# Optimization experiments

Measured on AMD Instinct MI355X. Metric: run time of the kernel, lower is better.

The kernel has to match this reference:

```python
import jax, jax.numpy as jnp
import numpy as np
from jax import lax

B, N, D, H, K = 8, 1024, 384, 6, 7
HD = D // H
EPS = 1e-5


def layer_norm(x, g, b):
    m = jnp.mean(x, axis=-1, keepdims=True)
    v = jnp.mean(jnp.square(x - m), axis=-1, keepdims=True)
    return (x - m) * lax.rsqrt(v + EPS) * g + b


def setup_inputs() -> dict:
    key = jax.random.key(0)
    ks = jax.random.split(key, 12)
    s = 0.02
    return {
        "x": jax.random.normal(ks[0], (B, N, D), jnp.float32),
        "qkv_w": jax.random.normal(ks[1], (3 * D, D), jnp.float32) * s,
        "qkv_b": jnp.zeros((3 * D,), jnp.float32),
        "proj_w": jax.random.normal(ks[2], (D, D), jnp.float32) * s,
        "proj_b": jnp.zeros((D,), jnp.float32),
        "t_before": jnp.eye(H, dtype=jnp.float32) + jax.random.normal(ks[3], (H, H), jnp.float32) * 0.01,
        "t_after": jnp.eye(H, dtype=jnp.float32) + jax.random.normal(ks[4], (H, H), jnp.float32) * 0.01,
        "dw_w": jax.random.normal(ks[5], (D, 1, K), jnp.float32) * s,
        "dw_b": jnp.zeros((D,), jnp.float32),
        "mlp_ln_g": jnp.ones((D,), jnp.float32),
        "mlp_ln_b": jnp.zeros((D,), jnp.float32),
        "norm1_g": jnp.ones((D,), jnp.float32),
        "norm1_b": jnp.zeros((D,), jnp.float32),
        "norm2_g": jnp.ones((D,), jnp.float32),
        "norm2_b": jnp.zeros((D,), jnp.float32),
        "fc1_w": jax.random.normal(ks[6], (4 * D, D), jnp.float32) * s,
        "fc1_b": jnp.zeros((4 * D,), jnp.float32),
        "fc2_w": jax.random.normal(ks[7], (D, 4 * D), jnp.float32) * s,
        "fc2_b": jnp.zeros((D,), jnp.float32),
    }


def reference(x, qkv_w, qkv_b, proj_w, proj_b, t_before, t_after, dw_w, dw_b,
              mlp_ln_g, mlp_ln_b, norm1_g, norm1_b, norm2_g, norm2_b,
              fc1_w, fc1_b, fc2_w, fc2_b):
    # ---- attention branch ----
    h = layer_norm(x, norm1_g, norm1_b)
    qkv = h @ qkv_w.T + qkv_b                                  # (B,N,3D)
    qkv = qkv.reshape(B, N, 3, H, HD).transpose(2, 0, 3, 1, 4)  # (3,B,H,N,hd)
    q, k, v = qkv[0], qkv[1], qkv[2]
    scale = HD ** -0.5
    scores = jnp.einsum('bhnd,bhmd->bhnm', q, k) * scale        # (B,H,N,N)
    scores = jnp.einsum('gh,bhnm->bgnm', t_before, scores)       # head-mix pre-softmax
    probs = jax.nn.softmax(scores, axis=-1)
    probs = jnp.einsum('gh,bhnm->bgnm', t_after, probs)          # head-mix post-softmax
    attn_out = jnp.einsum('bhnm,bhmd->bhnd', probs, v)           # (B,H,N,hd)
    attn_out = attn_out.transpose(0, 2, 1, 3).reshape(B, N, D)
    attn_out = attn_out @ proj_w.T + proj_b
    x = x + attn_out
    # ---- MLP branch ----
    h = layer_norm(x, norm2_g, norm2_b)
    # depthwise conv1d over tokens: (B,D,N), groups=D, same padding
    h_t = h.transpose(0, 2, 1)
    h_t = lax.conv_general_dilated(h_t, dw_w, window_strides=(1,),
                                   padding=[(K // 2, K // 2)],
                                   dimension_numbers=('NCH', 'OIH', 'NCH'),
                                   feature_group_count=D)
    h = h_t.transpose(0, 2, 1) + dw_b
    h = layer_norm(h, mlp_ln_g, mlp_ln_b)
    h = jax.nn.gelu(h @ fc1_w.T + fc1_b, approximate=False)
    h = h @ fc2_w.T + fc2_b
    return x + h
```

## Files before the change

### kernel.cpp

```cpp
#include <hip/hip_runtime.h>
#include <hip/hip_bf16.h>

#define BB 8
#define NN 1024
#define DD 384
#define HH 6
#define HD 64
#define BN 8192
#define D3 1152
#define D4 1536
#define SEC 3145728

typedef __attribute__((ext_vector_type(8))) short short8;
typedef __attribute__((ext_vector_type(4))) float f32x4;
typedef __attribute__((ext_vector_type(2))) float f32x2;
typedef long v2i64 __attribute__((ext_vector_type(2)));

typedef __attribute__((address_space(3))) unsigned char as3_byte;
typedef __attribute__((address_space(1))) const unsigned char as1_byte;

__device__ __forceinline__ void gload16(const void* g, void* l){
  __builtin_amdgcn_global_load_lds((as1_byte*)g, (as3_byte*)l, 16, 0, 0);
}

__device__ __forceinline__ float b2f(unsigned short u){
  union{unsigned int i; float f;} x; x.i=((unsigned int)u)<<16; return x.f;
}
__device__ __forceinline__ unsigned short f2b(float f){
  unsigned int u=__float_as_uint(f);
  return (unsigned short)((u + 0x7FFFu + ((u>>16)&1u))>>16);
}

__global__ void cvt_kernel(const float* __restrict__ w0, const float* __restrict__ w1,
                           const float* __restrict__ w2, const float* __restrict__ w3,
                           unsigned short* __restrict__ out){
  int i = blockIdx.x*256 + threadIdx.x;
  if (i < 442368)        out[i] = f2b(w0[i]);
  else if (i < 589824)   out[i] = f2b(w1[i - 442368]);
  else if (i < 1179648)  out[i] = f2b(w2[i - 589824]);
  else if (i < 1769472)  out[i] = f2b(w3[i - 1179648]);
}

__global__ __launch_bounds__(128)
void ln_kernel(const float* __restrict__ in, const float* __restrict__ gg, const float* __restrict__ bb,
               unsigned short* __restrict__ outb){
  int row = blockIdx.x, t = threadIdx.x;
  const float* r = in + (size_t)row*DD;
  float v0=r[t], v1=r[t+128], v2=r[t+256];
  float s=v0+v1+v2, q=v0*v0+v1*v1+v2*v2;
  #pragma unroll
  for (int o=32;o>0;o>>=1){ s+=__shfl_down(s,o); q+=__shfl_down(q,o); }
  __shared__ float ls[2], lq[2];
  if ((t&63)==0){ ls[t>>6]=s; lq[t>>6]=q; }
  __syncthreads();
  float S=ls[0]+ls[1], Q=lq[0]+lq[1];
  float mean=S*(1.0f/DD);
  float rstd=rsqrtf(Q*(1.0f/DD)-mean*mean+1e-5f);
  unsigned short* o=outb+(size_t)row*DD;
  o[t]    =f2b((v0-mean)*rstd*gg[t]+bb[t]);
  o[t+128]=f2b((v1-mean)*rstd*gg[t+128]+bb[t+128]);
  o[t+256]=f2b((v2-mean)*rstd*gg[t+256]+bb[t+256]);
}

__global__ __launch_bounds__(128)
void conv_ln_kernel(const unsigned short* __restrict__ h2, const float* __restrict__ dww, const float* __restrict__ dwb,
                    const float* __restrict__ gg, const float* __restrict__ bb, unsigned short* __restrict__ out){
  int row=blockIdx.x, t=threadIdx.x;
  int bi=row>>10, n=row&1023;
  const unsigned short* base = h2 + (size_t)(bi<<10)*DD;
  float a[3];
  #pragma unroll
  for (int j=0;j<3;j++){
    int d=t+j*128;
    float acc=dwb[d];
    #pragma unroll
    for (int k=0;k<7;k++){
      int nn=n+k-3;
      if (nn>=0 && nn<NN) acc += dww[d*7+k]*b2f(base[(size_t)nn*DD + d]);
    }
    a[j]=acc;
  }
  float s=a[0]+a[1]+a[2], q=a[0]*a[0]+a[1]*a[1]+a[2]*a[2];
  #pragma unroll
  for (int o=32;o>0;o>>=1){ s+=__shfl_down(s,o); q+=__shfl_down(q,o); }
  __shared__ float ls[2], lq[2];
  if ((t&63)==0){ ls[t>>6]=s; lq[t>>6]=q; }
  __syncthreads();
  float S=ls[0]+ls[1], Q=lq[0]+lq[1];
  float mean=S*(1.0f/DD);
  float rstd=rsqrtf(Q*(1.0f/DD)-mean*mean+1e-5f);
  unsigned short* o = out + (size_t)row*DD;
  #pragma unroll
  for (int j=0;j<3;j++){
    int d=t+j*128;
    o[d]=f2b((a[j]-mean)*rstd*gg[d]+bb[d]);
  }
}

template<int MODE, int TN>
__global__ __launch_bounds__(256)
void gemm_kernel(const unsigned short* __restrict__ A, const unsigned short* __restrict__ W,
                 const float* __restrict__ bias, const float* __restrict__ resid,
                 float* __restrict__ outf, unsigned short* __restrict__ outb,
                 unsigned char* __restrict__ qk8out, unsigned char* __restrict__ v8out,
                 int Kdim, int Ncols){
  constexpr int JF = TN/32;
  __shared__ __align__(16) unsigned short lds_a[2][128*32];
  __shared__ __align__(16) unsigned short lds_b[2][TN*32];
  int t=threadIdx.x, lane=t&63, w=t>>6;
  int bm = blockIdx.x*128;
  int bn = blockIdx.y*TN;
  int wr = w>>1, wc = w&1;
  int rm = lane&15, r16 = lane>>4;
  f32x4 acc[4][JF] = {};
  char* ldsa_c = (char*)lds_a;
  char* ldsb_c = (char*)lds_b;
  int abyte[4], bbyte[JF];
  #pragma unroll
  for (int i=0;i<4;i++){
    int ra = wr*64 + i*16 + rm;
    abyte[i] = ra*64 + ((r16 ^ ((ra>>1)&3))*16);
  }
  #pragma unroll
  for (int j=0;j<JF;j++){
    int rb = wc*(TN/2) + j*16 + rm;
    bbyte[j] = rb*64 + ((r16 ^ ((rb>>1)&3))*16);
  }
  auto stage = [&](int buf, int k0){
    #pragma unroll
    for (int c=0;c<2;c++){
      int u = t + c*256;
      int row = u>>2, sl = (u&3) ^ ((row>>1)&3);
      gload16(A + (size_t)(bm+row)*Kdim + k0 + sl*8, ldsa_c + buf*8192 + u*16);
    }
    #pragma unroll
    for (int c=0;c<TN/64;c++){
      int u = t + c*256;
      int row = u>>2, sl = (u&3) ^ ((row>>1)&3);
      gload16(W + (size_t)(bn+row)*Kdim + k0 + sl*8, ldsb_c + buf*(TN*64) + u*16);
    }
  };
  int niter = Kdim>>5;
  stage(0, 0);
  __syncthreads();
  for (int it=0; it<niter; ++it){
    if (it+1<niter) stage((it+1)&1, (it+1)<<5);
    int ab = (it&1)*8192, bb2 = (it&1)*(TN*64);
    short8 af[4], bf[JF];
    #pragma unroll
    for (int i=0;i<4;i++) af[i]=*reinterpret_cast<const short8*>(ldsa_c + ab + abyte[i]);
    #pragma unroll
    for (int j=0;j<JF;j++) bf[j]=*reinterpret_cast<const short8*>(ldsb_c + bb2 + bbyte[j]);
    #pragma unroll
    for (int i=0;i<4;i++)
      #pragma unroll
      for (int j=0;j<JF;j++)
        acc[i][j]=__builtin_amdgcn_mfma_f32_16x16x32_bf16(af[i],bf[j],acc[i][j],0,0,0);
    __syncthreads();
  }
  #pragma unroll
  for (int i=0;i<4;i++){
    #pragma unroll
    for (int j=0;j<JF;j++){
      #pragma unroll
      for (int r=0;r<4;r++){
        int row = bm + wr*64 + i*16 + r16*4 + r;
        int col = bn + wc*(TN/2) + j*16 + rm;
        float v = acc[i][j][r] + bias[col];
        if (MODE==0){
          int c = col/384; int rem = col - c*384; int hh = rem>>6, d = rem&63;
          int bi = row>>10, nn = row&1023;
          unsigned char pk = (unsigned char)(__builtin_amdgcn_cvt_pk_fp8_f32(v, v, 0, false) & 0xff);
          if (c==2){
            v8out[(((size_t)(bi*6+hh))<<16) + ((size_t)d<<10) + nn] = pk;
          } else {
            size_t fa = ((size_t)c*SEC)
                      + ((((size_t)(bi*6+hh))<<6) + (nn>>4))*1024
                      + ((((d>>3)&3)*16 + (nn&15))<<4) + ((d>>5)*8) + (d&7);
            qk8out[fa] = pk;
          }
        } else if (MODE==1){
          size_t idx = (size_t)row*Ncols + col;
          outf[idx] = resid[idx] + v;
        } else {
          float ge = 0.5f*v*(1.0f+erff(v*0.70710678118654752f));
          outb[(size_t)row*Ncols + col] = f2b(ge);
        }
      }
    }
  }
}

__global__ __launch_bounds__(256, 4)
void smx_kernel(const unsigned char* __restrict__ qk8, const float* __restrict__ tbm,
                unsigned char* __restrict__ E, float* __restrict__ lpart){
  __shared__ float lred[4][6][16];
  int t=threadIdx.x, lane=t&63, w=t>>6;
  int blk=blockIdx.x;
  int b = blk&7, nt = (blk>>3)&63, mh = blk>>9;
  int n0 = nt*16, mbase = mh*512;
  int c16=lane&15, r16=lane>>4;
  const unsigned char* q8f = qk8;
  const unsigned char* k8f = qk8 + SEC;
  v2i64 qf[6];
  #pragma unroll
  for (int h=0;h<6;h++)
    qf[h] = *(const v2i64*)(q8f + (((((size_t)(b*6+h))<<6) + (n0>>4))<<10) + lane*16);
  float tbr[36];
  #pragma unroll
  for (int i=0;i<36;i++) tbr[i] = tbm[i];
  const float SC = 0.125f*1.44269504088896f;
  float lsum[6]={0.f,0.f,0.f,0.f,0.f,0.f};
  #pragma unroll
  for (int mt=0; mt<4; ++mt){
    int m0a = mbase + mt*128 + w*16;
    int m0b = m0a + 64;
    v2i64 kfa[6], kfb[6];
    #pragma unroll
    for (int h=0;h<6;h++)
      kfa[h] = *(const v2i64*)(k8f + (((((size_t)(b*6+h))<<6) + (m0a>>4))<<10) + lane*16);
    #pragma unroll
    for (int h=0;h<6;h++)
      kfb[h] = *(const v2i64*)(k8f + (((((size_t)(b*6+h))<<6) + (m0b>>4))<<10) + lane*16);
    {
      f32x4 aq[6] = {};
      #pragma unroll
      for (int h=0;h<6;h++){
        aq[h] = __builtin_amdgcn_mfma_f32_16x16x32_fp8_fp8(kfa[h][0], qf[h][0], aq[h], 0,0,0);
        aq[h] = __builtin_amdgcn_mfma_f32_16x16x32_fp8_fp8(kfa[h][1], qf[h][1], aq[h], 0,0,0);
      }
      #pragma unroll
      for (int g=0;g<6;g++){
        float e0,e1,e2,e3;
        {
          float sm;
          sm = tbr[g*6]*aq[0][0]+tbr[g*6+1]*aq[1][0]+tbr[g*6+2]*aq[2][0]
             + tbr[g*6+3]*aq[3][0]+tbr[g*6+4]*aq[4][0]+tbr[g*6+5]*aq[5][0];
          e0 = __builtin_amdgcn_exp2f(sm*SC);
          sm = tbr[g*6]*aq[0][1]+tbr[g*6+1]*aq[1][1]+tbr[g*6+2]*aq[2][1]
             + tbr[g*6+3]*aq[3][1]+tbr[g*6+4]*aq[4][1]+tbr[g*6+5]*aq[5][1];
          e1 = __builtin_amdgcn_exp2f(sm*SC);
          sm = tbr[g*6]*aq[0][2]+tbr[g*6+1]*aq[1][2]+tbr[g*6+2]*aq[2][2]
             + tbr[g*6+3]*aq[3][2]+tbr[g*6+4]*aq[4][2]+tbr[g*6+5]*aq[5][2];
          e2 = __builtin_amdgcn_exp2f(sm*SC);
          sm = tbr[g*6]*aq[0][3]+tbr[g*6+1]*aq[1][3]+tbr[g*6+2]*aq[2][3]
             + tbr[g*6+3]*aq[3][3]+tbr[g*6+4]*aq[4][3]+tbr[g*6+5]*aq[5][3];
          e3 = __builtin_amdgcn_exp2f(sm*SC);
        }
        lsum[g] += (e0+e1)+(e2+e3);
        int pkv = __builtin_amdgcn_cvt_pk_fp8_f32(e0, e1, 0, false);
        pkv = __builtin_amdgcn_cvt_pk_fp8_f32(e2, e3, pkv, true);
        *(unsigned int*)(E + (((size_t)(b*6+g))<<20) + ((size_t)(n0+c16)<<10) + m0a + r16*4)
          = (unsigned int)pkv;
      }
    }
    {
      f32x4 aq[6] = {};
      #pragma unroll
      for (int h=0;h<6;h++){
        aq[h] = __builtin_amdgcn_mfma_f32_16x16x32_fp8_fp8(kfb[h][0], qf[h][0], aq[h], 0,0,0);
        aq[h] = __builtin_amdgcn_mfma_f32_16x16x32_fp8_fp8(kfb[h][1], qf[h][1], aq[h], 0,0,0);
      }
      #pragma unroll
      for (int g=0;g<6;g++){
        float e0,e1,e2,e3;
        {
          float sm;
          sm = tbr[g*6]*aq[0][0]+tbr[g*6+1]*aq[1][0]+tbr[g*6+2]*aq[2][0]
             + tbr[g*6+3]*aq[3][0]+tbr[g*6+4]*aq[4][0]+tbr[g*6+5]*aq[5][0];
          e0 = __builtin_amdgcn_exp2f(sm*SC);
          sm = tbr[g*6]*aq[0][1]+tbr[g*6+1]*aq[1][1]+tbr[g*6+2]*aq[2][1]
             + tbr[g*6+3]*aq[3][1]+tbr[g*6+4]*aq[4][1]+tbr[g*6+5]*aq[5][1];
          e1 = __builtin_amdgcn_exp2f(sm*SC);
          sm = tbr[g*6]*aq[0][2]+tbr[g*6+1]*aq[1][2]+tbr[g*6+2]*aq[2][2]
             + tbr[g*6+3]*aq[3][2]+tbr[g*6+4]*aq[4][2]+tbr[g*6+5]*aq[5][2];
          e2 = __builtin_amdgcn_exp2f(sm*SC);
          sm = tbr[g*6]*aq[0][3]+tbr[g*6+1]*aq[1][3]+tbr[g*6+2]*aq[2][3]
             + tbr[g*6+3]*aq[3][3]+tbr[g*6+4]*aq[4][3]+tbr[g*6+5]*aq[5][3];
          e3 = __builtin_amdgcn_exp2f(sm*SC);
        }
        lsum[g] += (e0+e1)+(e2+e3);
        int pkv = __builtin_amdgcn_cvt_pk_fp8_f32(e0, e1, 0, false);
        pkv = __builtin_amdgcn_cvt_pk_fp8_f32(e2, e3, pkv, true);
        *(unsigned int*)(E + (((size_t)(b*6+g))<<20) + ((size_t)(n0+c16)<<10) + m0b + r16*4)
          = (unsigned int)pkv;
      }
    }
  }
  #pragma unroll
  for (int g=0;g<6;g++){
    lsum[g] += __shfl_xor(lsum[g],16);
    lsum[g] += __shfl_xor(lsum[g],32);
  }
  if (r16==0){
    #pragma unroll
    for (int g=0;g<6;g++) lred[w][g][c16] = lsum[g];
  }
  __syncthreads();
  if (w==0 && r16==0){
    #pragma unroll
    for (int g=0;g<6;g++){
      float l = lred[0][g][c16]+lred[1][g][c16]+lred[2][g][c16]+lred[3][g][c16];
      lpart[(((size_t)(mh*48 + b*6+g))<<10) + n0 + c16] = l;
    }
  }
}

__global__ __launch_bounds__(256, 2)
void pvmix_kernel(const unsigned char* __restrict__ E, const unsigned char* __restrict__ V8,
                  const float* __restrict__ lpart, const float* __restrict__ tam,
                  unsigned short* __restrict__ outp){
  __shared__ __align__(16) unsigned char Es[6*16*64];
  __shared__ __align__(16) unsigned char Vs[6*64*64];
  __shared__ __align__(16) unsigned char pms[6*16*64];
  int t=threadIdx.x, lane=t&63, w=t>>6;
  int b = blockIdx.x&7, nt = blockIdx.x>>3;
  int n0 = nt*16;
  int c16 = lane&15, r16 = lane>>4;
  int mn = t&15, mg = (t>>4)&7, gh = t>>7;
  float cf[3][6];
  #pragma unroll
  for (int g=0;g<6;g++){
    float l0 = lpart[(((size_t)(b*6+g))<<10) + n0 + mn];
    float l1 = lpart[(((size_t)(48 + b*6+g))<<10) + n0 + mn];
    float iv = 256.0f/(l0 + l1);
    #pragma unroll
    for (int j=0;j<3;j++) cf[j][g] = tam[(gh*3+j)*6 + g]*iv;
  }
  auto stageE = [&](int m0){
    #pragma unroll
    for (int i=0;i<2;i++){
      int u = t + i*256;
      if (u<384){
        int r = u>>2, s = (u&3) ^ (r&3);
        int g = r>>4, n = r&15;
        gload16(E + (((size_t)(b*6+g))<<20) + ((size_t)(n0+n)<<10) + m0 + s*16,
                (char*)Es + u*16);
      }
    }
  };
  auto stageV = [&](int m0){
    #pragma unroll
    for (int i=0;i<6;i++){
      int u = t + i*256;
      int r = u>>2, s = (u&3) ^ (r&3);
      int g = r>>6, d = r&63;
      gload16(V8 + (((size_t)(b*6+g))<<16) + ((size_t)d<<10) + m0 + s*16,
              (char*)Vs + u*16);
    }
  };
  stageE(0); stageV(0);
  __syncthreads();
  f32x4 acc[6] = {};
  for (int mt=0; mt<16; ++mt){
    float e[6][8];
    #pragma unroll
    for (int g=0;g<6;g++){
      int row = g*16 + mn;
      int byteo = row*64 + ((mg*8) ^ ((row&3)<<4));
      unsigned int lo = *(const unsigned int*)(Es + byteo);
      unsigned int hi = *(const unsigned int*)(Es + byteo + 4);
      f32x2 p0 = __builtin_amdgcn_cvt_pk_f32_fp8(lo, false);
      f32x2 p1 = __builtin_amdgcn_cvt_pk_f32_fp8(lo, true);
      f32x2 p2 = __builtin_amdgcn_cvt_pk_f32_fp8(hi, false);
      f32x2 p3 = __builtin_amdgcn_cvt_pk_f32_fp8(hi, true);
      e[g][0]=p0.x; e[g][1]=p0.y; e[g][2]=p1.x; e[g][3]=p1.y;
      e[g][4]=p2.x; e[g][5]=p2.y; e[g][6]=p3.x; e[g][7]=p3.y;
    }
    #pragma unroll
    for (int j=0;j<3;j++){
      float pm[8];
      #pragma unroll
      for (int m=0;m<8;m++)
        pm[m] = cf[j][0]*e[0][m]+cf[j][1]*e[1][m]+cf[j][2]*e[2][m]
              + cf[j][3]*e[3][m]+cf[j][4]*e[4][m]+cf[j][5]*e[5][m];
      int d0 = __builtin_amdgcn_cvt_pk_fp8_f32(pm[0], pm[1], 0, false);
      d0 = __builtin_amdgcn_cvt_pk_fp8_f32(pm[2], pm[3], d0, true);
      int d1 = __builtin_amdgcn_cvt_pk_fp8_f32(pm[4], pm[5], 0, false);
      d1 = __builtin_amdgcn_cvt_pk_fp8_f32(pm[6], pm[7], d1, true);
      int prow = (gh*3+j)*16 + mn;
      int pbyte = prow*64 + ((mg*8) ^ ((mn&7)<<3));
      *(unsigned int*)(pms + pbyte)     = (unsigned int)d0;
      *(unsigned int*)(pms + pbyte + 4) = (unsigned int)d1;
    }
    __syncthreads();
    if (mt<15) stageE((mt+1)*64);
    #pragma unroll
    for (int g=0;g<6;g++){
      int arow = g*16 + c16;
      int vrow = g*64 + w*16 + c16;
      #pragma unroll
      for (int kk=0;kk<2;kk++){
        long af = *(const long*)(pms + arow*64 + ((kk*32 + r16*8) ^ ((c16&7)<<3)));
        long bf = *(const long*)(Vs + vrow*64
                   + ((((kk*2 + (r16>>1)) ^ (vrow&3))<<4) + ((r16&1)<<3)));
        acc[g] = __builtin_amdgcn_mfma_f32_16x16x32_fp8_fp8(af, bf, acc[g], 0,0,0);
      }
    }
    __syncthreads();
    if (mt<15) stageV((mt+1)*64);
  }
  #pragma unroll
  for (int g=0;g<6;g++)
    #pragma unroll
    for (int r=0;r<4;r++){
      int n = n0 + r16*4 + r;
      int d = g*64 + w*16 + c16;
      outp[((size_t)(b*1024 + n))*DD + d] = f2b(acc[g][r] * 0.00390625f);
    }
}

extern "C" void kernel_launch(void* const* d_in, const int* in_sizes, int n_in,
                              void* d_out, int out_size, void* d_ws, size_t ws_size,
                              hipStream_t stream){
  const float* x      = (const float*)d_in[0];
  const float* qkv_w  = (const float*)d_in[1];
  const float* qkv_b  = (const float*)d_in[2];
  const float* proj_w = (const float*)d_in[3];
  const float* proj_b = (const float*)d_in[4];
  const float* t_before=(const float*)d_in[5];
  const float* t_after =(const float*)d_in[6];
  const float* dw_w   = (const float*)d_in[7];
  const float* dw_b   = (const float*)d_in[8];
  const float* mlp_g  = (const float*)d_in[9];
  const float* mlp_b  = (const float*)d_in[10];
  const float* n1_g   = (const float*)d_in[11];
  const float* n1_b   = (const float*)d_in[12];
  const float* n2_g   = (const float*)d_in[13];
  const float* n2_b   = (const float*)d_in[14];
  const float* fc1_w  = (const float*)d_in[15];
  const float* fc1_b  = (const float*)d_in[16];
  const float* fc2_w  = (const float*)d_in[17];
  const float* fc2_b  = (const float*)d_in[18];
  float* out = (float*)d_out;
  char* ws = (char*)d_ws;
  unsigned short* qkvwb = (unsigned short*)(ws + 0);
  unsigned short* projwb= (unsigned short*)(ws + 884736);
  unsigned short* fc1wb = (unsigned short*)(ws + 1179648);
  unsigned short* fc2wb = (unsigned short*)(ws + 2359296);
  unsigned short* hb    = (unsigned short*)(ws + 3538944);
  unsigned char*  qk8   = (unsigned char*) (ws + 9830400);
  unsigned char*  V8    = (unsigned char*) (ws + 28704768);
  float*          lpart = (float*)        (ws + 31850496);
  unsigned char*  Ebuf  = (unsigned char*) (ws + 34996224);
  unsigned short* attnb = (unsigned short*)(ws + 85327872);
  float*          x2    = (float*)(ws + 91619328);
  unsigned short* h2 = (unsigned short*)qk8;
  unsigned short* hcln = hb;
  unsigned short* fc1o = (unsigned short*)Ebuf;

  cvt_kernel<<<6912,256,0,stream>>>(qkv_w, proj_w, fc1_w, fc2_w, qkvwb);

  ln_kernel<<<BN,128,0,stream>>>(x, n1_g, n1_b, hb);
  { dim3 g(BN/128, D3/128); gemm_kernel<0,128><<<g,256,0,stream>>>(hb, qkvwb, qkv_b, nullptr, nullptr, nullptr, qk8, V8, DD, D3); }
  smx_kernel<<<1024,256,0,stream>>>(qk8, t_before, Ebuf, lpart);
  pvmix_kernel<<<512,256,0,stream>>>(Ebuf, V8, lpart, t_after, attnb);
  { dim3 g(BN/128, DD/64); gemm_kernel<1,64><<<g,256,0,stream>>>(attnb, projwb, proj_b, x, x2, nullptr, nullptr, nullptr, DD, DD); }
  ln_kernel<<<BN,128,0,stream>>>(x2, n2_g, n2_b, h2);
  conv_ln_kernel<<<BN,128,0,stream>>>(h2, dw_w, dw_b, mlp_g, mlp_b, hcln);
  { dim3 g(BN/128, D4/128); gemm_kernel<2,128><<<g,256,0,stream>>>(hcln, fc1wb, fc1_b, nullptr, nullptr, fc1o, nullptr, nullptr, DD, D4); }
  { dim3 g(BN/128, DD/64); gemm_kernel<1,64><<<g,256,0,stream>>>(fc1o, fc2wb, fc2_b, x2, out, nullptr, nullptr, nullptr, D4, DD); }
}
```

Baseline: 192.9 us.

## Run MLP GEMMs in FP8 with scaled activations and weights

Converts fc1/fc2 weights, the conv+LN output and the GELU output to FP8 with fixed power-of-two scales, and adds a new 64x64-tile FP8 MFMA GEMM kernel that replaces the bf16 GEMMs for both MLP matmuls. This halves operand bytes and uses the higher-throughput fp8 MFMA path. The risk is accuracy loss from FP8 quantisation of activations and weights, and the smaller tiles give less data reuse per block.

Result: faster. 187.7 us (-2.7%).

```diff
diff --git a/kernel.cpp b/kernel.cpp
--- a/kernel.cpp
+++ b/kernel.cpp
@@ -30,15 +30,18 @@
   unsigned int u=__float_as_uint(f);
   return (unsigned short)((u + 0x7FFFu + ((u>>16)&1u))>>16);
 }
+__device__ __forceinline__ unsigned char f2f8(float f){
+  return (unsigned char)(__builtin_amdgcn_cvt_pk_fp8_f32(f, f, 0, false) & 0xff);
+}
 
 __global__ void cvt_kernel(const float* __restrict__ w0, const float* __restrict__ w1,
                            const float* __restrict__ w2, const float* __restrict__ w3,
-                           unsigned short* __restrict__ out){
+                           unsigned short* __restrict__ outb, unsigned char* __restrict__ out8){
   int i = blockIdx.x*256 + threadIdx.x;
-  if (i < 442368)        out[i] = f2b(w0[i]);
-  else if (i < 589824)   out[i] = f2b(w1[i - 442368]);
-  else if (i < 1179648)  out[i] = f2b(w2[i - 589824]);
-  else if (i < 1769472)  out[i] = f2b(w3[i - 1179648]);
+  if (i < 442368)        outb[i] = f2b(w0[i]);
+  else if (i < 589824)   outb[i] = f2b(w1[i - 442368]);
+  else if (i < 1179648)  out8[i - 589824] = f2f8(w2[i - 589824]*8.0f);
+  else if (i < 1769472)  out8[i - 589824] = f2f8(w3[i - 1179648]*8.0f);
 }
 
 __global__ __launch_bounds__(128)
@@ -64,7 +67,7 @@
 
 __global__ __launch_bounds__(128)
 void conv_ln_kernel(const unsigned short* __restrict__ h2, const float* __restrict__ dww, const float* __restrict__ dwb,
-                    const float* __restrict__ gg, const float* __restrict__ bb, unsigned short* __restrict__ out){
+                    const float* __restrict__ gg, const float* __restrict__ bb, unsigned char* __restrict__ out8){
   int row=blockIdx.x, t=threadIdx.x;
   int bi=row>>10, n=row&1023;
   const unsigned short* base = h2 + (size_t)(bi<<10)*DD;
@@ -89,11 +92,11 @@
   float S=ls[0]+ls[1], Q=lq[0]+lq[1];
   float mean=S*(1.0f/DD);
   float rstd=rsqrtf(Q*(1.0f/DD)-mean*mean+1e-5f);
-  unsigned short* o = out + (size_t)row*DD;
+  unsigned char* o = out8 + (size_t)row*DD;
   #pragma unroll
   for (int j=0;j<3;j++){
     int d=t+j*128;
-    o[d]=f2b((a[j]-mean)*rstd*gg[d]+bb[d]);
+    o[d]=f2f8(((a[j]-mean)*rstd*gg[d]+bb[d])*4.0f);
   }
 }
 
@@ -101,7 +104,7 @@
 __global__ __launch_bounds__(256)
 void gemm_kernel(const unsigned short* __restrict__ A, const unsigned short* __restrict__ W,
                  const float* __restrict__ bias, const float* __restrict__ resid,
-                 float* __restrict__ outf, unsigned short* __restrict__ outb,
+                 float* __restrict__ outf,
                  unsigned char* __restrict__ qk8out, unsigned char* __restrict__ v8out,
                  int Kdim, int Ncols){
   constexpr int JF = TN/32;
@@ -170,7 +173,7 @@
         if (MODE==0){
           int c = col/384; int rem = col - c*384; int hh = rem>>6, d = rem&63;
           int bi = row>>10, nn = row&1023;
-          unsigned char pk = (unsigned char)(__builtin_amdgcn_cvt_pk_fp8_f32(v, v, 0, false) & 0xff);
+          unsigned char pk = f2f8(v);
           if (c==2){
             v8out[(((size_t)(bi*6+hh))<<16) + ((size_t)d<<10) + nn] = pk;
           } else {
@@ -179,16 +182,77 @@
                       + ((((d>>3)&3)*16 + (nn&15))<<4) + ((d>>5)*8) + (d&7);
             qk8out[fa] = pk;
           }
-        } else if (MODE==1){
+        } else {
+          size_t idx = (size_t)row*Ncols + col;
+          outf[idx] = resid[idx] + v;
+        }
+      }
+    }
+  }
+}
+
+template<int MODE>
+__global__ __launch_bounds__(256)
+void gemm8_kernel(const unsigned char* __restrict__ A8, const unsigned char* __restrict__ W8,
+                  const float* __restrict__ bias, const float* __restrict__ resid,
+                  float* __restrict__ outf, unsigned char* __restrict__ out8,
+                  int Kdim, int Ncols){
+  __shared__ __align__(16) unsigned char As[2][64*64];
+  __shared__ __align__(16) unsigned char Bs[2][64*64];
+  int t=threadIdx.x, lane=t&63, w=t>>6;
+  int bm = blockIdx.x*64;
+  int bn = blockIdx.y*64;
+  int wr = w>>1, wc = w&1;
+  int c16=lane&15, r16=lane>>4;
+  f32x4 acc[2][2] = {};
+  int arow = t>>2, aslot = (t&3) ^ (arow&3);
+  auto stage = [&](int buf, int k0){
+    gload16(A8 + (size_t)(bm+arow)*Kdim + k0 + aslot*16, (char*)As + buf*4096 + t*16);
+    gload16(W8 + (size_t)(bn+arow)*Kdim + k0 + aslot*16, (char*)Bs + buf*4096 + t*16);
+  };
+  int niter = Kdim>>6;
+  stage(0, 0);
+  __syncthreads();
+  for (int it=0; it<niter; ++it){
+    if (it+1<niter) stage((it+1)&1, (it+1)<<6);
+    int off = (it&1)*4096;
+    #pragma unroll
+    for (int kk=0;kk<2;kk++){
+      long afr[2], bfr[2];
+      #pragma unroll
+      for (int i=0;i<2;i++){
+        int ra = wr*32 + i*16 + c16;
+        int sa = (kk*2 + (r16>>1)) ^ (ra&3);
+        afr[i] = *(const long*)((char*)As + off + ra*64 + (sa<<4) + ((r16&1)<<3));
+        int rb = wc*32 + i*16 + c16;
+        int sb = (kk*2 + (r16>>1)) ^ (rb&3);
+        bfr[i] = *(const long*)((char*)Bs + off + rb*64 + (sb<<4) + ((r16&1)<<3));
+      }
+      #pragma unroll
+      for (int i=0;i<2;i++)
+        #pragma unroll
+        for (int j=0;j<2;j++)
+          acc[i][j] = __builtin_amdgcn_mfma_f32_16x16x32_fp8_fp8(afr[i], bfr[j], acc[i][j], 0,0,0);
+    }
+    __syncthreads();
+  }
+  #pragma unroll
+  for (int i=0;i<2;i++)
+    #pragma unroll
+    for (int j=0;j<2;j++)
+      #pragma unroll
+      for (int r=0;r<4;r++){
+        int row = bm + wr*32 + i*16 + r16*4 + r;
+        int col = bn + wc*32 + j*16 + c16;
+        float v = acc[i][j][r]*0.03125f + bias[col];
+        if (MODE==1){
           size_t idx = (size_t)row*Ncols + col;
           outf[idx] = resid[idx] + v;
         } else {
           float ge = 0.5f*v*(1.0f+erff(v*0.70710678118654752f));
-          outb[(size_t)row*Ncols + col] = f2b(ge);
+          out8[(size_t)row*Ncols + col] = f2f8(ge*4.0f);
         }
       }
-    }
-  }
 }
 
 __global__ __launch_bounds__(256, 4)
@@ -436,28 +500,28 @@
   char* ws = (char*)d_ws;
   unsigned short* qkvwb = (unsigned short*)(ws + 0);
   unsigned short* projwb= (unsigned short*)(ws + 884736);
-  unsigned short* fc1wb = (unsigned short*)(ws + 1179648);
-  unsigned short* fc2wb = (unsigned short*)(ws + 2359296);
-  unsigned short* hb    = (unsigned short*)(ws + 3538944);
-  unsigned char*  qk8   = (unsigned char*) (ws + 9830400);
-  unsigned char*  V8    = (unsigned char*) (ws + 28704768);
-  float*          lpart = (float*)        (ws + 31850496);
-  unsigned char*  Ebuf  = (unsigned char*) (ws + 34996224);
-  unsigned short* attnb = (unsigned short*)(ws + 85327872);
-  float*          x2    = (float*)(ws + 91619328);
+  unsigned char*  fc1w8 = (unsigned char*) (ws + 1179648);
+  unsigned char*  fc2w8 = (unsigned char*) (ws + 1769472);
+  unsigned short* hb    = (unsigned short*)(ws + 2359296);
+  unsigned char*  qk8   = (unsigned char*) (ws + 8650752);
+  unsigned char*  V8    = (unsigned char*) (ws + 27525120);
+  float*          lpart = (float*)        (ws + 30670848);
+  unsigned char*  Ebuf  = (unsigned char*) (ws + 31064064);
+  unsigned short* attnb = (unsigned short*)(ws + 81395712);
+  float*          x2    = (float*)(ws + 87687168);
   unsigned short* h2 = (unsigned short*)qk8;
-  unsigned short* hcln = hb;
-  unsigned short* fc1o = (unsigned short*)Ebuf;
-
-  cvt_kernel<<<6912,256,0,stream>>>(qkv_w, proj_w, fc1_w, fc2_w, qkvwb);
+  unsigned char*  hcln8 = (unsigned char*)hb;
+  unsigned char*  fc1o8 = Ebuf;
+
+  cvt_kernel<<<6912,256,0,stream>>>(qkv_w, proj_w, fc1_w, fc2_w, qkvwb, fc1w8);
 
   ln_kernel<<<BN,128,0,stream>>>(x, n1_g, n1_b, hb);
-  { dim3 g(BN/128, D3/128); gemm_kernel<0,128><<<g,256,0,stream>>>(hb, qkvwb, qkv_b, nullptr, nullptr, nullptr, qk8, V8, DD, D3); }
+  { dim3 g(BN/128, D3/128); gemm_kernel<0,128><<<g,256,0,stream>>>(hb, qkvwb, qkv_b, nullptr, nullptr, qk8, V8, DD, D3); }
   smx_kernel<<<1024,256,0,stream>>>(qk8, t_before, Ebuf, lpart);
   pvmix_kernel<<<512,256,0,stream>>>(Ebuf, V8, lpart, t_after, attnb);
-  { dim3 g(BN/128, DD/64); gemm_kernel<1,64><<<g,256,0,stream>>>(attnb, projwb, proj_b, x, x2, nullptr, nullptr, nullptr, DD, DD); }
+  { dim3 g(BN/128, DD/64); gemm_kernel<1,64><<<g,256,0,stream>>>(attnb, projwb, proj_b, x, x2, nullptr, nullptr, DD, DD); }
   ln_kernel<<<BN,128,0,stream>>>(x2, n2_g, n2_b, h2);
-  conv_ln_kernel<<<BN,128,0,stream>>>(h2, dw_w, dw_b, mlp_g, mlp_b, hcln);
-  { dim3 g(BN/128, D4/128); gemm_kernel<2,128><<<g,256,0,stream>>>(hcln, fc1wb, fc1_b, nullptr, nullptr, fc1o, nullptr, nullptr, DD, D4); }
-  { dim3 g(BN/128, DD/64); gemm_kernel<1,64><<<g,256,0,stream>>>(fc1o, fc2wb, fc2_b, x2, out, nullptr, nullptr, nullptr, D4, DD); }
-}
+  conv_ln_kernel<<<BN,128,0,stream>>>(h2, dw_w, dw_b, mlp_g, mlp_b, hcln8);
+  { dim3 g(BN/64, D4/64); gemm8_kernel<2><<<g,256,0,stream>>>(hcln8, fc1w8, fc1_b, nullptr, nullptr, fc1o8, DD, D4); }
+  { dim3 g(BN/64, DD/64); gemm8_kernel<1><<<g,256,0,stream>>>(fc1o8, fc2w8, fc2_b, x2, out, nullptr, D4, DD); }
+}
```
